# Kernel optimization log

Measured on AMD Instinct MI355X. Metric: run time of the kernel, lower is better.

## Reference

```python
import jax, jax.numpy as jnp
import numpy as np

N_NODES = 50000
N_EDGES = 800000
IN_DIM = 1280
HID = 512
EMB = 64
LN_EPS = 1e-5
NEG_SLOPE = 0.2  # DGL GATConv default leaky_relu slope


def setup_inputs() -> dict:
    key = jax.random.key(0)
    ks = jax.random.split(key, 10)
    features = jax.random.normal(ks[0], (N_NODES, IN_DIM), dtype=jnp.float32)
    src = jax.random.randint(ks[1], (N_EDGES,), 0, N_NODES)
    dst = jax.random.randint(ks[2], (N_EDGES,), 0, N_NODES)
    # MLPBlock params: Linear(IN_DIM -> HID) + LayerNorm(HID)
    W1 = jax.random.normal(ks[3], (IN_DIM, HID), dtype=jnp.float32) / np.sqrt(IN_DIM)
    b1 = jnp.zeros((HID,), dtype=jnp.float32)
    ln_g = jnp.ones((HID,), dtype=jnp.float32)
    ln_b = jnp.zeros((HID,), dtype=jnp.float32)
    # GATConv params (num_heads=1): fc (no bias), attn_l, attn_r, output bias
    Wg = jax.random.normal(ks[4], (HID, EMB), dtype=jnp.float32) / np.sqrt(HID)
    attn_l = jax.random.normal(ks[5], (EMB,), dtype=jnp.float32) * 0.1
    attn_r = jax.random.normal(ks[6], (EMB,), dtype=jnp.float32) * 0.1
    bias_g = jnp.zeros((EMB,), dtype=jnp.float32)
    return {"features": features, "src": src, "dst": dst, "W1": W1, "b1": b1,
            "ln_g": ln_g, "ln_b": ln_b, "Wg": Wg, "attn_l": attn_l,
            "attn_r": attn_r, "bias_g": bias_g}


def reference(features, src, dst, W1, b1, ln_g, ln_b, Wg, attn_l, attn_r, bias_g):
    # MLPBlock: linear -> ReLU -> LayerNorm (dropout is identity in eval)
    x = jax.nn.relu(features @ W1 + b1)                     # [N, HID]
    mu = jnp.mean(x, axis=-1, keepdims=True)
    var = jnp.mean(jnp.square(x - mu), axis=-1, keepdims=True)
    x = (x - mu) * jax.lax.rsqrt(var + LN_EPS) * ln_g + ln_b

    # GATConv (single head)
    feat = x @ Wg                                           # [N, EMB]
    el = feat @ attn_l                                      # [N]
    er = feat @ attn_r                                      # [N]
    e = jax.nn.leaky_relu(el[src] + er[dst], NEG_SLOPE)     # [E]

    # edge softmax over incoming edges of each dst node
    m = jax.ops.segment_max(e, dst, num_segments=N_NODES)   # [N]
    ex = jnp.exp(e - m[dst])                                # [E]
    s = jax.ops.segment_sum(ex, dst, num_segments=N_NODES)  # [N]
    a = ex / s[dst]                                         # [E]

    # scatter-aggregate weighted source features
    out = jax.ops.segment_sum(a[:, None] * feat[src], dst, num_segments=N_NODES)
    return out + bias_g                                     # [N, EMB] (head dim squeezed)
```

## Files before the change

### kernel.cpp

```cpp
#include <hip/hip_runtime.h>
#include <hip/hip_bf16.h>
#include <stdint.h>

#define N_NODES 50000
#define N_EDGES 800000
#define IN_DIM 1280
#define HID 512
#define EMB 64
#define M_PAD 50048
#define MT1 391
#define LN_EPS 1e-5f

typedef __attribute__((ext_vector_type(8))) __bf16 bf16x8;
typedef __attribute__((ext_vector_type(4))) float floatx4;

#define AS1C(p) ((const __attribute__((address_space(1))) void*)(p))
#define AS3(p)  ((__attribute__((address_space(3))) void*)(p))

__device__ __forceinline__ unsigned f2bf(float f) {
  unsigned u = __float_as_uint(f);
  u += 0x7FFFu + ((u >> 16) & 1u);
  return u >> 16;
}
__device__ __forceinline__ float bf2f(unsigned short s) {
  return __uint_as_float(((unsigned)s) << 16);
}

__global__ __launch_bounds__(256) void k_prep(const float* __restrict__ W1,
                                              const float* __restrict__ Wg,
                                              const float* __restrict__ ln_g,
                                              const float* __restrict__ ln_b,
                                              unsigned short* __restrict__ B1t,
                                              unsigned short* __restrict__ Wgp,
                                              float* __restrict__ uvec,
                                              float* __restrict__ vvec,
                                              int* __restrict__ deg,
                                              float* __restrict__ s1,
                                              float* __restrict__ s2) {
  int idx = blockIdx.x * 256 + threadIdx.x;
  if (idx < HID * IN_DIM) {
    int n = idx / IN_DIM;
    int k = idx - n * IN_DIM;
    B1t[idx] = (unsigned short)f2bf(W1[(size_t)k * HID + n]);
  }
  if (idx < EMB * HID) {
    int n = idx >> 9;
    int k = idx & 511;
    Wgp[idx] = (unsigned short)f2bf(ln_g[k] * Wg[(size_t)k * EMB + n]);
  }
  if (idx < EMB) {
    float su = 0.f, sv = 0.f;
    for (int k = 0; k < HID; ++k) {
      float wv = Wg[(size_t)k * EMB + idx];
      su += ln_b[k] * wv;
      sv += ln_g[k] * wv;
    }
    uvec[idx] = su;
    vvec[idx] = sv;
  }
  if (idx < N_NODES) deg[idx] = 0;
  if (idx < M_PAD) { s1[idx] = 0.f; s2[idx] = 0.f; }
}

__global__ __launch_bounds__(256) void k_convhist(const float* __restrict__ F,
                                                  unsigned short* __restrict__ Fb,
                                                  const int* __restrict__ dst,
                                                  int* __restrict__ deg) {
  if (blockIdx.x < 31280) {
    size_t base = ((size_t)blockIdx.x * 256 + threadIdx.x) * 8;
    uint4 o;
    if (base < (size_t)N_NODES * IN_DIM) {
      float4 f0 = *(const float4*)(F + base);
      float4 f1 = *(const float4*)(F + base + 4);
      o.x = f2bf(f0.x) | (f2bf(f0.y) << 16);
      o.y = f2bf(f0.z) | (f2bf(f0.w) << 16);
      o.z = f2bf(f1.x) | (f2bf(f1.y) << 16);
      o.w = f2bf(f1.z) | (f2bf(f1.w) << 16);
    } else {
      o = make_uint4(0u, 0u, 0u, 0u);
    }
    *(uint4*)(Fb + base) = o;
  } else {
    int t = (blockIdx.x - 31280) * 256 + threadIdx.x;
    if (t < N_EDGES) atomicAdd(&deg[dst[t]], 1);
  }
}

__global__ __launch_bounds__(256) void k_gemm1(const unsigned short* __restrict__ Abf,
                                               const unsigned short* __restrict__ Bt,
                                               const float* __restrict__ bias1,
                                               unsigned short* __restrict__ xn,
                                               float* __restrict__ s1,
                                               float* __restrict__ s2) {
  __shared__ unsigned short As[128 * 64];
  __shared__ unsigned short Bs[128 * 64];
  const int t = threadIdx.x;
  const int o = blockIdx.x;
  const int xcd = o & 7, pos = o >> 3;
  const int lin = (xcd < 4 ? xcd * 196 : 784 + (xcd - 4) * 195) + pos;
  const int bm = lin >> 2, bn = lin & 3;
  const int w = t >> 6, lane = t & 63, quad = lane >> 4, lr = lane & 15;
  const int wm = (w & 1) * 64, wn = (w >> 1) * 64;

  floatx4 acc[4][4];
#pragma unroll
  for (int i = 0; i < 4; ++i)
#pragma unroll
    for (int j = 0; j < 4; ++j) acc[i][j] = (floatx4){0.f, 0.f, 0.f, 0.f};

  const int rr = t >> 3;
  const int cc = (t & 7) ^ (rr & 7);
  const unsigned short* aP[4];
  const unsigned short* bP[4];
#pragma unroll
  for (int j = 0; j < 4; ++j) {
    aP[j] = Abf + (size_t)(bm * 128 + j * 32 + rr) * IN_DIM + cc * 8;
    bP[j] = Bt + (size_t)(bn * 128 + j * 32 + rr) * IN_DIM + cc * 8;
  }
  unsigned short* asw = As + w * 512;
  unsigned short* bsw = Bs + w * 512;

  const int l7 = lr & 7;

  for (int k0 = 0; k0 < IN_DIM; k0 += 64) {
#pragma unroll
    for (int j = 0; j < 4; ++j) {
      __builtin_amdgcn_global_load_lds(AS1C(aP[j] + k0), AS3(asw + j * 2048), 16, 0, 0);
      __builtin_amdgcn_global_load_lds(AS1C(bP[j] + k0), AS3(bsw + j * 2048), 16, 0, 0);
    }
    __syncthreads();

#pragma unroll
    for (int h = 0; h < 2; ++h) {
      const int col = ((h * 4 + quad) ^ l7) * 8;
      bf16x8 af[4], bfv[4];
#pragma unroll
      for (int mi = 0; mi < 4; ++mi)
        af[mi] = *(const bf16x8*)&As[(wm + mi * 16 + lr) * 64 + col];
#pragma unroll
      for (int ni = 0; ni < 4; ++ni)
        bfv[ni] = *(const bf16x8*)&Bs[(wn + ni * 16 + lr) * 64 + col];
#pragma unroll
      for (int mi = 0; mi < 4; ++mi)
#pragma unroll
        for (int ni = 0; ni < 4; ++ni)
          acc[mi][ni] = __builtin_amdgcn_mfma_f32_16x16x32_bf16(af[mi], bfv[ni], acc[mi][ni], 0, 0, 0);
    }
    __syncthreads();
  }

#pragma unroll
  for (int mi = 0; mi < 4; ++mi) {
    int gr = bm * 128 + wm + mi * 16 + quad * 4;
#pragma unroll
    for (int r = 0; r < 4; ++r) {
      float ps1 = 0.f, ps2 = 0.f;
#pragma unroll
      for (int ni = 0; ni < 4; ++ni) {
        int gc = bn * 128 + wn + ni * 16 + lr;
        float v = acc[mi][ni][r] + bias1[gc];
        v = v > 0.f ? v : 0.f;
        unsigned short h = (unsigned short)f2bf(v);
        xn[(size_t)(gr + r) * HID + gc] = h;
        float vr = bf2f(h);
        ps1 += vr;
        ps2 += vr * vr;
      }
#pragma unroll
      for (int m = 1; m < 16; m <<= 1) {
        ps1 += __shfl_xor(ps1, m, 64);
        ps2 += __shfl_xor(ps2, m, 64);
      }
      if (lr == 0) {
        atomicAdd(&s1[gr + r], ps1);
        atomicAdd(&s2[gr + r], ps2);
      }
    }
  }
}

__device__ __forceinline__ int swz(int r) { return (r ^ (r >> 2)) & 3; }

__global__ __launch_bounds__(256) void k_gemm2(const unsigned short* __restrict__ Xn,
                                               const unsigned short* __restrict__ Wgp,
                                               const float* __restrict__ s1,
                                               const float* __restrict__ s2,
                                               const float* __restrict__ uvec,
                                               const float* __restrict__ vvec,
                                               const float* __restrict__ al,
                                               const float* __restrict__ ar,
                                               float* __restrict__ feat,
                                               float* __restrict__ el,
                                               float* __restrict__ er) {
  __shared__ unsigned short As[128 * 32];
  __shared__ unsigned short Bs[64 * 32];
  const int t = threadIdx.x;
  const int bm = blockIdx.x;
  const int w = t >> 6, lane = t & 63, quad = lane >> 4, lr = lane & 15;

  floatx4 acc[2][4];
#pragma unroll
  for (int i = 0; i < 2; ++i)
#pragma unroll
    for (int j = 0; j < 4; ++j) acc[i][j] = (floatx4){0.f, 0.f, 0.f, 0.f};

  const int r0 = t >> 2, c0 = (t & 3) ^ swz(t >> 2);
  const int r1 = 64 + (t >> 2), c1 = (t & 3) ^ swz(64 + (t >> 2));
  const unsigned short* a0 = Xn + (size_t)(bm * 128 + r0) * HID + c0 * 8;
  const unsigned short* a1 = Xn + (size_t)(bm * 128 + r1) * HID + c1 * 8;
  const unsigned short* b0 = Wgp + (size_t)r0 * HID + c0 * 8;
  unsigned short* asw = As + w * 512;
  unsigned short* bsw = Bs + w * 512;

  const int q2 = quad ^ swz(lr);

  for (int k0 = 0; k0 < HID; k0 += 32) {
    __builtin_amdgcn_global_load_lds(AS1C(a0 + k0), AS3(asw), 16, 0, 0);
    __builtin_amdgcn_global_load_lds(AS1C(a1 + k0), AS3(asw + 2048), 16, 0, 0);
    __builtin_amdgcn_global_load_lds(AS1C(b0 + k0), AS3(bsw), 16, 0, 0);
    __syncthreads();

    bf16x8 af[2], bfv[4];
#pragma unroll
    for (int mi = 0; mi < 2; ++mi)
      af[mi] = *(const bf16x8*)&As[(w * 32 + mi * 16 + lr) * 32 + q2 * 8];
#pragma unroll
    for (int ni = 0; ni < 4; ++ni)
      bfv[ni] = *(const bf16x8*)&Bs[(ni * 16 + lr) * 32 + q2 * 8];
#pragma unroll
    for (int mi = 0; mi < 2; ++mi)
#pragma unroll
      for (int ni = 0; ni < 4; ++ni)
        acc[mi][ni] = __builtin_amdgcn_mfma_f32_16x16x32_bf16(af[mi], bfv[ni], acc[mi][ni], 0, 0, 0);
    __syncthreads();
  }

  float alv[4], arv[4], uv[4], vv[4];
#pragma unroll
  for (int ni = 0; ni < 4; ++ni) {
    alv[ni] = al[ni * 16 + lr];
    arv[ni] = ar[ni * 16 + lr];
    uv[ni] = uvec[ni * 16 + lr];
    vv[ni] = vvec[ni * 16 + lr];
  }
#pragma unroll
  for (int mi = 0; mi < 2; ++mi) {
    int gr = bm * 128 + w * 32 + mi * 16 + quad * 4;
#pragma unroll
    for (int r = 0; r < 4; ++r) {
      int row = gr + r;
      float mu = s1[row] * (1.f / HID);
      float rs = rsqrtf(s2[row] * (1.f / HID) - mu * mu + LN_EPS);
      float mrs = mu * rs;
      float sl = 0.f, sr2 = 0.f;
#pragma unroll
      for (int ni = 0; ni < 4; ++ni) {
        float v = rs * acc[mi][ni][r] + uv[ni] - mrs * vv[ni];
        feat[(size_t)row * EMB + ni * 16 + lr] = v;
        sl += v * alv[ni];
        sr2 += v * arv[ni];
      }
#pragma unroll
      for (int m = 1; m < 16; m <<= 1) {
        sl += __shfl_xor(sl, m, 64);
        sr2 += __shfl_xor(sr2, m, 64);
      }
      if (lr == 0) {
        el[row] = sl;
        er[row] = sr2;
      }
    }
  }
}

__global__ __launch_bounds__(256) void k_scan1(const int* __restrict__ deg,
                                               int* __restrict__ rowstart,
                                               int* __restrict__ bsum) {
  __shared__ int sh[256];
  int t = threadIdx.x, i = blockIdx.x * 256 + t;
  int x = (i < N_NODES) ? deg[i] : 0;
  sh[t] = x;
  __syncthreads();
  for (int off = 1; off < 256; off <<= 1) {
    int v = (t >= off) ? sh[t - off] : 0;
    __syncthreads();
    sh[t] += v;
    __syncthreads();
  }
  if (i < N_NODES) rowstart[i] = sh[t] - x;
  if (t == 255) bsum[blockIdx.x] = sh[255];
}

__global__ __launch_bounds__(256) void k_scan23(const int* __restrict__ bsum,
                                                int* __restrict__ rowstart,
                                                int* __restrict__ cursor) {
  __shared__ int sh[256];
  int t = threadIdx.x;
  int x = (t < 196) ? bsum[t] : 0;
  sh[t] = x;
  __syncthreads();
  for (int off = 1; off < 256; off <<= 1) {
    int v = (t >= off) ? sh[t - off] : 0;
    __syncthreads();
    sh[t] += v;
    __syncthreads();
  }
  int boff = (blockIdx.x > 0) ? sh[blockIdx.x - 1] : 0;
  __syncthreads();
  int i = blockIdx.x * 256 + t;
  if (i < N_NODES) {
    int rs = rowstart[i] + boff;
    rowstart[i] = rs;
    cursor[i] = rs;
  }
}

__global__ __launch_bounds__(256) void k_fill(const int* __restrict__ src,
                                              const int* __restrict__ dst,
                                              int* __restrict__ cursor,
                                              int* __restrict__ csr_src) {
  int t = blockIdx.x * 256 + threadIdx.x;
  if (t >= N_EDGES) return;
  int pos = atomicAdd(&cursor[dst[t]], 1);
  csr_src[pos] = src[t];
}

__global__ __launch_bounds__(256) void k_gat(const int* __restrict__ rowstart,
                                             const int* __restrict__ deg,
                                             const int* __restrict__ csr_src,
                                             const float* __restrict__ el,
                                             const float* __restrict__ er,
                                             const float* __restrict__ feat,
                                             const float* __restrict__ bias_g,
                                             float* __restrict__ out) {
  int w = threadIdx.x >> 6, lane = threadIdx.x & 63;
  int v = blockIdx.x * 4 + w;
  int start = rowstart[v], d = deg[v];
  float erv = er[v];
  float s = 0.f, O = 0.f;
#pragma unroll 4
  for (int i = 0; i < d; ++i) {
    int sv = csr_src[start + i];
    float f = feat[(size_t)sv * EMB + lane];
    float e = el[sv] + erv;
    e = e > 0.f ? e : 0.2f * e;
    float p = __expf(e);
    s += p;
    O = fmaf(p, f, O);
  }
  out[(size_t)v * EMB + lane] = (d > 0 ? O / s : 0.f) + bias_g[lane];
}

extern "C" void kernel_launch(void* const* d_in, const int* in_sizes, int n_in,
                              void* d_out, int out_size, void* d_ws, size_t ws_size,
                              hipStream_t stream) {
  const float* features = (const float*)d_in[0];
  const int* src        = (const int*)d_in[1];
  const int* dst        = (const int*)d_in[2];
  const float* W1       = (const float*)d_in[3];
  const float* b1       = (const float*)d_in[4];
  const float* ln_g     = (const float*)d_in[5];
  const float* ln_b     = (const float*)d_in[6];
  const float* Wg       = (const float*)d_in[7];
  const float* attn_l   = (const float*)d_in[8];
  const float* attn_r   = (const float*)d_in[9];
  const float* bias_g   = (const float*)d_in[10];
  float* out = (float*)d_out;

  char* ws = (char*)d_ws;
  size_t off = 0;
  auto alloc = [&](size_t bytes) {
    char* p = ws + off;
    off = (off + bytes + 255) & ~(size_t)255;
    return p;
  };
  unsigned short* B1t   = (unsigned short*)alloc((size_t)HID * IN_DIM * 2);
  unsigned short* Wgp   = (unsigned short*)alloc((size_t)EMB * HID * 2);
  unsigned short* featbf= (unsigned short*)alloc((size_t)M_PAD * IN_DIM * 2);
  unsigned short* xn    = (unsigned short*)alloc((size_t)M_PAD * HID * 2);
  float* feat           = (float*)alloc((size_t)M_PAD * EMB * 4);
  float* el             = (float*)alloc((size_t)M_PAD * 4);
  float* er             = (float*)alloc((size_t)M_PAD * 4);
  float* s1             = (float*)alloc((size_t)M_PAD * 4);
  float* s2             = (float*)alloc((size_t)M_PAD * 4);
  float* uvec           = (float*)alloc(EMB * 4);
  float* vvec           = (float*)alloc(EMB * 4);
  int* deg              = (int*)alloc((size_t)N_NODES * 4);
  int* rowstart         = (int*)alloc((size_t)N_NODES * 4);
  int* cursor           = (int*)alloc((size_t)N_NODES * 4);
  int* bsum             = (int*)alloc(256 * 4);
  int* csr_src          = (int*)alloc((size_t)N_EDGES * 4);
  (void)ws_size; (void)in_sizes; (void)n_in; (void)out_size;

  k_prep<<<dim3(2560), dim3(256), 0, stream>>>(W1, Wg, ln_g, ln_b, B1t, Wgp,
                                               uvec, vvec, deg, s1, s2);
  k_convhist<<<dim3(31280 + 3125), dim3(256), 0, stream>>>(features, featbf, dst, deg);
  k_scan1<<<dim3(196), dim3(256), 0, stream>>>(deg, rowstart, bsum);
  k_scan23<<<dim3(196), dim3(256), 0, stream>>>(bsum, rowstart, cursor);
  k_fill<<<dim3(3125), dim3(256), 0, stream>>>(src, dst, cursor, csr_src);
  k_gemm1<<<dim3(1564), dim3(256), 0, stream>>>(featbf, B1t, b1, xn, s1, s2);
  k_gemm2<<<dim3(MT1), dim3(256), 0, stream>>>(xn, Wgp, s1, s2, uvec, vvec,
                                               attn_l, attn_r, feat, el, er);
  k_gat<<<dim3(12500), dim3(256), 0, stream>>>(rowstart, deg, csr_src, el, er, feat, bias_g, out);
}
```

Baseline: 688.7 us.

## Pipeline GEMM1 with 256x128 tiles, triple-buffered LDS and phased MFMA scheduling

The first GEMM moves from 128x128 tiles with 4 waves to 256x128 tiles with 8 waves, so each block stages more A rows per shared B tile. A is triple-buffered and B double-buffered in 128 KB of dynamic LDS, and global-to-LDS loads for later k-steps are issued in between the MFMA phases. Raised MFMA priority and explicit vmcnt waits replace the two full syncthreads per k-step. Padding grows to a multiple of 256 rows, which adds some wasted conversion and compute, and the large LDS footprint limits how many blocks fit per CU.

```diff
diff --git a/kernel.cpp b/kernel.cpp
--- a/kernel.cpp
+++ b/kernel.cpp
@@ -7,7 +7,7 @@
 #define IN_DIM 1280
 #define HID 512
 #define EMB 64
-#define M_PAD 50048
+#define M_PAD 50176
 #define MT1 391
 #define LN_EPS 1e-5f
 
@@ -66,7 +66,7 @@
                                                   unsigned short* __restrict__ Fb,
                                                   const int* __restrict__ dst,
                                                   int* __restrict__ deg) {
-  if (blockIdx.x < 31280) {
+  if (blockIdx.x < 31360) {
     size_t base = ((size_t)blockIdx.x * 256 + threadIdx.x) * 8;
     uint4 o;
     if (base < (size_t)N_NODES * IN_DIM) {
@@ -81,26 +81,26 @@
     }
     *(uint4*)(Fb + base) = o;
   } else {
-    int t = (blockIdx.x - 31280) * 256 + threadIdx.x;
+    int t = (blockIdx.x - 31360) * 256 + threadIdx.x;
     if (t < N_EDGES) atomicAdd(&deg[dst[t]], 1);
   }
 }
 
-__global__ __launch_bounds__(256) void k_gemm1(const unsigned short* __restrict__ Abf,
-                                               const unsigned short* __restrict__ Bt,
-                                               const float* __restrict__ bias1,
-                                               unsigned short* __restrict__ xn,
-                                               float* __restrict__ s1,
-                                               float* __restrict__ s2) {
-  __shared__ unsigned short As[128 * 64];
-  __shared__ unsigned short Bs[128 * 64];
+__global__ __launch_bounds__(512, 2) void k_gemm1(const unsigned short* __restrict__ Abf,
+                                                  const unsigned short* __restrict__ Bt,
+                                                  const float* __restrict__ bias1,
+                                                  unsigned short* __restrict__ xn,
+                                                  float* __restrict__ s1,
+                                                  float* __restrict__ s2) {
+  extern __shared__ char smem[];
   const int t = threadIdx.x;
   const int o = blockIdx.x;
-  const int xcd = o & 7, pos = o >> 3;
-  const int lin = (xcd < 4 ? xcd * 196 : 784 + (xcd - 4) * 195) + pos;
+  const int lin = (o & 7) * 98 + (o >> 3);
   const int bm = lin >> 2, bn = lin & 3;
   const int w = t >> 6, lane = t & 63, quad = lane >> 4, lr = lane & 15;
-  const int wm = (w & 1) * 64, wn = (w >> 1) * 64;
+  const int wm = (w >> 1) * 64;
+  const int wn = (w & 1) * 64;
+  const int l7 = lr & 7;
 
   floatx4 acc[4][4];
 #pragma unroll
@@ -111,47 +111,131 @@
   const int rr = t >> 3;
   const int cc = (t & 7) ^ (rr & 7);
   const unsigned short* aP[4];
-  const unsigned short* bP[4];
-#pragma unroll
-  for (int j = 0; j < 4; ++j) {
-    aP[j] = Abf + (size_t)(bm * 128 + j * 32 + rr) * IN_DIM + cc * 8;
-    bP[j] = Bt + (size_t)(bn * 128 + j * 32 + rr) * IN_DIM + cc * 8;
-  }
-  unsigned short* asw = As + w * 512;
-  unsigned short* bsw = Bs + w * 512;
-
-  const int l7 = lr & 7;
-
-  for (int k0 = 0; k0 < IN_DIM; k0 += 64) {
-#pragma unroll
-    for (int j = 0; j < 4; ++j) {
-      __builtin_amdgcn_global_load_lds(AS1C(aP[j] + k0), AS3(asw + j * 2048), 16, 0, 0);
-      __builtin_amdgcn_global_load_lds(AS1C(bP[j] + k0), AS3(bsw + j * 2048), 16, 0, 0);
-    }
-    __syncthreads();
-
-#pragma unroll
-    for (int h = 0; h < 2; ++h) {
-      const int col = ((h * 4 + quad) ^ l7) * 8;
-      bf16x8 af[4], bfv[4];
+  const unsigned short* bP[2];
+#pragma unroll
+  for (int j = 0; j < 4; ++j)
+    aP[j] = Abf + (size_t)(bm * 256 + j * 64 + rr) * IN_DIM + cc * 8;
+#pragma unroll
+  for (int j = 0; j < 2; ++j)
+    bP[j] = Bt + (size_t)(bn * 128 + j * 64 + rr) * IN_DIM + cc * 8;
+  const int stoff = w * 1024;
+
+#define GL(gp, lp) __builtin_amdgcn_global_load_lds(AS1C(gp), AS3(lp), 16, 0, 0)
+#define STAGE_A_FULL(k0, b3) do { \
+    GL(aP[0] + (k0), smem + (b3) * 32768 + 0 * 8192 + stoff); \
+    GL(aP[1] + (k0), smem + (b3) * 32768 + 1 * 8192 + stoff); \
+    GL(aP[2] + (k0), smem + (b3) * 32768 + 2 * 8192 + stoff); \
+    GL(aP[3] + (k0), smem + (b3) * 32768 + 3 * 8192 + stoff); } while (0)
+#define STAGE_A_H0(k0, b3) do { \
+    GL(aP[0] + (k0), smem + (b3) * 32768 + 0 * 8192 + stoff); \
+    GL(aP[1] + (k0), smem + (b3) * 32768 + 1 * 8192 + stoff); } while (0)
+#define STAGE_A_H1(k0, b3) do { \
+    GL(aP[2] + (k0), smem + (b3) * 32768 + 2 * 8192 + stoff); \
+    GL(aP[3] + (k0), smem + (b3) * 32768 + 3 * 8192 + stoff); } while (0)
+#define STAGE_B2(k0, b2) do { \
+    GL(bP[0] + (k0), smem + 98304 + (b2) * 16384 + 0 * 8192 + stoff); \
+    GL(bP[1] + (k0), smem + 98304 + (b2) * 16384 + 1 * 8192 + stoff); } while (0)
+#define PH_IN() do { asm volatile("" ::: "memory"); __builtin_amdgcn_s_barrier(); \
+    asm volatile("s_waitcnt lgkmcnt(0)" ::: "memory"); \
+    __builtin_amdgcn_sched_barrier(0); } while (0)
+#define PH_OUT() do { asm volatile("" ::: "memory"); __builtin_amdgcn_s_barrier(); } while (0)
+#define MFMA(a, b, c) __builtin_amdgcn_mfma_f32_16x16x32_bf16((a), (b), (c), 0, 0, 0)
+
+  STAGE_A_FULL(0, 0);
+  STAGE_B2(0, 0);
+  STAGE_A_FULL(64, 1);
+  asm volatile("s_waitcnt vmcnt(4)" ::: "memory");
+  __builtin_amdgcn_s_barrier();
+  asm volatile("" ::: "memory");
+
+  for (int it = 0; it < 20; ++it) {
+    const unsigned short* Ab = (const unsigned short*)(smem + (it % 3) * 32768);
+    const unsigned short* Bb = (const unsigned short*)(smem + 98304 + (it & 1) * 16384);
+    const int k2 = (it + 2) * 64;
+    bf16x8 af[4], b0, b1;
+    {
+      const int cq = (quad ^ l7) * 8;
 #pragma unroll
       for (int mi = 0; mi < 4; ++mi)
-        af[mi] = *(const bf16x8*)&As[(wm + mi * 16 + lr) * 64 + col];
-#pragma unroll
-      for (int ni = 0; ni < 4; ++ni)
-        bfv[ni] = *(const bf16x8*)&Bs[(wn + ni * 16 + lr) * 64 + col];
+        af[mi] = *(const bf16x8*)&Ab[(wm + mi * 16 + lr) * 64 + cq];
+      b0 = *(const bf16x8*)&Bb[(wn + 0 * 16 + lr) * 64 + cq];
+      b1 = *(const bf16x8*)&Bb[(wn + 1 * 16 + lr) * 64 + cq];
+      if (it + 1 < 20) STAGE_B2((it + 1) * 64, (it + 1) & 1);
+      PH_IN();
+      __builtin_amdgcn_s_setprio(1);
+#pragma unroll
+      for (int mi = 0; mi < 4; ++mi) {
+        acc[mi][0] = MFMA(af[mi], b0, acc[mi][0]);
+        acc[mi][1] = MFMA(af[mi], b1, acc[mi][1]);
+      }
+      __builtin_amdgcn_s_setprio(0);
+      PH_OUT();
+    }
+    {
+      const int cq = (quad ^ l7) * 8;
+      b0 = *(const bf16x8*)&Bb[(wn + 2 * 16 + lr) * 64 + cq];
+      b1 = *(const bf16x8*)&Bb[(wn + 3 * 16 + lr) * 64 + cq];
+      if (it + 2 < 20) STAGE_A_H0(k2, (it + 2) % 3);
+      PH_IN();
+      __builtin_amdgcn_s_setprio(1);
+#pragma unroll
+      for (int mi = 0; mi < 4; ++mi) {
+        acc[mi][2] = MFMA(af[mi], b0, acc[mi][2]);
+        acc[mi][3] = MFMA(af[mi], b1, acc[mi][3]);
+      }
+      __builtin_amdgcn_s_setprio(0);
+      PH_OUT();
+    }
+    {
+      const int cq = ((4 + quad) ^ l7) * 8;
 #pragma unroll
       for (int mi = 0; mi < 4; ++mi)
-#pragma unroll
-        for (int ni = 0; ni < 4; ++ni)
-          acc[mi][ni] = __builtin_amdgcn_mfma_f32_16x16x32_bf16(af[mi], bfv[ni], acc[mi][ni], 0, 0, 0);
-    }
-    __syncthreads();
-  }
+        af[mi] = *(const bf16x8*)&Ab[(wm + mi * 16 + lr) * 64 + cq];
+      b0 = *(const bf16x8*)&Bb[(wn + 0 * 16 + lr) * 64 + cq];
+      b1 = *(const bf16x8*)&Bb[(wn + 1 * 16 + lr) * 64 + cq];
+      if (it + 2 < 20) STAGE_A_H1(k2, (it + 2) % 3);
+      PH_IN();
+      __builtin_amdgcn_s_setprio(1);
+#pragma unroll
+      for (int mi = 0; mi < 4; ++mi) {
+        acc[mi][0] = MFMA(af[mi], b0, acc[mi][0]);
+        acc[mi][1] = MFMA(af[mi], b1, acc[mi][1]);
+      }
+      __builtin_amdgcn_s_setprio(0);
+      PH_OUT();
+    }
+    {
+      const int cq = ((4 + quad) ^ l7) * 8;
+      b0 = *(const bf16x8*)&Bb[(wn + 2 * 16 + lr) * 64 + cq];
+      b1 = *(const bf16x8*)&Bb[(wn + 3 * 16 + lr) * 64 + cq];
+      PH_IN();
+      __builtin_amdgcn_s_setprio(1);
+#pragma unroll
+      for (int mi = 0; mi < 4; ++mi) {
+        acc[mi][2] = MFMA(af[mi], b0, acc[mi][2]);
+        acc[mi][3] = MFMA(af[mi], b1, acc[mi][3]);
+      }
+      __builtin_amdgcn_s_setprio(0);
+      if (it < 18) {
+        asm volatile("s_waitcnt vmcnt(4)" ::: "memory");
+      } else if (it == 18) {
+        asm volatile("s_waitcnt vmcnt(0)" ::: "memory");
+      }
+      PH_OUT();
+    }
+  }
+#undef GL
+#undef STAGE_A_FULL
+#undef STAGE_A_H0
+#undef STAGE_A_H1
+#undef STAGE_B2
+#undef PH_IN
+#undef PH_OUT
+#undef MFMA
 
 #pragma unroll
   for (int mi = 0; mi < 4; ++mi) {
-    int gr = bm * 128 + wm + mi * 16 + quad * 4;
+    int gr = bm * 256 + wm + mi * 16 + quad * 4;
 #pragma unroll
     for (int r = 0; r < 4; ++r) {
       float ps1 = 0.f, ps2 = 0.f;
@@ -392,13 +476,20 @@
   int* csr_src          = (int*)alloc((size_t)N_EDGES * 4);
   (void)ws_size; (void)in_sizes; (void)n_in; (void)out_size;
 
+  static int smem_set = 0;
+  if (!smem_set) {
+    hipFuncSetAttribute((const void*)k_gemm1,
+                        hipFuncAttributeMaxDynamicSharedMemorySize, 131072);
+    smem_set = 1;
+  }
+
   k_prep<<<dim3(2560), dim3(256), 0, stream>>>(W1, Wg, ln_g, ln_b, B1t, Wgp,
                                                uvec, vvec, deg, s1, s2);
-  k_convhist<<<dim3(31280 + 3125), dim3(256), 0, stream>>>(features, featbf, dst, deg);
+  k_convhist<<<dim3(31360 + 3125), dim3(256), 0, stream>>>(features, featbf, dst, deg);
   k_scan1<<<dim3(196), dim3(256), 0, stream>>>(deg, rowstart, bsum);
   k_scan23<<<dim3(196), dim3(256), 0, stream>>>(bsum, rowstart, cursor);
   k_fill<<<dim3(3125), dim3(256), 0, stream>>>(src, dst, cursor, csr_src);
-  k_gemm1<<<dim3(1564), dim3(256), 0, stream>>>(featbf, B1t, b1, xn, s1, s2);
+  k_gemm1<<<dim3(784), dim3(512), 131072, stream>>>(featbf, B1t, b1, xn, s1, s2);
   k_gemm2<<<dim3(MT1), dim3(256), 0, stream>>>(xn, Wgp, s1, s2, uvec, vvec,
                                                attn_l, attn_r, feat, el, er);
   k_gat<<<dim3(12500), dim3(256), 0, stream>>>(rowstart, deg, csr_src, el, er, feat, bias_g, out);
```

Result: faster. 654.4 us (-5.0%).
